# Performance work log

Hardware: AMD Instinct MI355X
Metric: run time of the kernel (lower is better)

The kernel has to match this reference:

```python
import jax, jax.numpy as jnp
import numpy as np
from jax import lax

LEAK = 0.2
GN_EPS = 1e-5
K_NEIGH = 16
GROUPS = 4


def knn_idx(coor_k, coor_q, k):
    # coor_k: [B,Nk,3], coor_q: [B,Nq,3] -> [B,Nq,k] indices of k nearest in coor_k
    d = (jnp.sum(coor_q * coor_q, -1, keepdims=True)
         - 2.0 * jnp.einsum('bqc,bkc->bqk', coor_q, coor_k)
         + jnp.sum(coor_k * coor_k, -1)[:, None, :])
    _, idx = lax.top_k(-d, k)
    return idx


def graph_feature(coor_q, x_q, coor_k, x_k, k):
    # coor_*: [B,3,N*]; x_q: [B,C,Nq]; x_k: [B,C,Nk] -> [B,2C,Nq,k]
    idx = knn_idx(lax.stop_gradient(coor_k).transpose(0, 2, 1),
                  lax.stop_gradient(coor_q).transpose(0, 2, 1), k)
    B = x_k.shape[0]
    x_k_t = x_k.transpose(0, 2, 1)                      # [B,Nk,C]
    b_idx = jnp.arange(B)[:, None, None]
    nb = x_k_t[b_idx, idx]                              # [B,Nq,k,C]
    nb = nb.transpose(0, 3, 1, 2)                       # [B,C,Nq,k]
    xq = x_q[:, :, :, None]                             # [B,C,Nq,1]
    return jnp.concatenate([nb - xq, jnp.broadcast_to(xq, nb.shape)], axis=1)


def conv_gn_lrelu_max(f, w, gamma, beta):
    # f: [B,Cin,N,k]; w: [Cout,Cin] -> [B,Cout,N] (max over k)
    y = jnp.einsum('oc,bcnk->bonk', w, f)
    B, C, N, Kk = y.shape
    g = y.reshape(B, GROUPS, C // GROUPS, N, Kk)
    mu = g.mean((2, 3, 4), keepdims=True)
    var = g.var((2, 3, 4), keepdims=True)
    g = (g - mu) * lax.rsqrt(var + GN_EPS)
    y = g.reshape(B, C, N, Kk) * gamma[None, :, None, None] + beta[None, :, None, None]
    y = jnp.where(y >= 0, y, LEAK * y)
    return y.max(axis=-1)


def fps(xyz, n):
    # xyz: [B,N,3] -> [B,n] int32 (furthest point sampling, start at index 0)
    B, N, _ = xyz.shape
    d0 = jnp.sum((xyz - xyz[:, :1]) ** 2, -1)           # dist to point 0
    def body(dist, _):
        idx = jnp.argmax(dist, -1)                       # [B]
        nxt = jnp.take_along_axis(xyz, idx[:, None, None], 1)
        dist = jnp.minimum(dist, jnp.sum((xyz - nxt) ** 2, -1))
        return dist, idx
    _, idxs = lax.scan(body, d0, None, length=n - 1)     # [n-1,B]
    first = jnp.zeros((1, B), idxs.dtype)
    return jnp.concatenate([first, idxs], 0).T           # [B,n]


def fps_downsample(coor, x, n):
    # coor: [B,3,N], x: [B,C,N] -> ([B,3,n], [B,C,n])
    idx = fps(lax.stop_gradient(coor).transpose(0, 2, 1), n)
    comb = jnp.concatenate([coor, x], axis=1)            # [B,3+C,N]
    b_idx = jnp.arange(coor.shape[0])[:, None]
    new = comb.transpose(0, 2, 1)[b_idx, idx].transpose(0, 2, 1)
    return new[:, :3], new[:, 3:]


def setup_inputs() -> dict:
    key = jax.random.key(0)
    ks = jax.random.split(key, 16)
    s = 0.1
    return {
        'x': jax.random.normal(ks[0], (32, 2048, 3), jnp.float32),
        'w_in': jax.random.normal(ks[1], (8, 3), jnp.float32) * s,
        'b_in': jnp.zeros((8,), jnp.float32),
        'w1': jax.random.normal(ks[2], (32, 16), jnp.float32) * s,
        'g1': jnp.ones((32,), jnp.float32), 'be1': jnp.zeros((32,), jnp.float32),
        'w2': jax.random.normal(ks[3], (64, 64), jnp.float32) * s,
        'g2': jnp.ones((64,), jnp.float32), 'be2': jnp.zeros((64,), jnp.float32),
        'w3': jax.random.normal(ks[4], (64, 128), jnp.float32) * s,
        'g3': jnp.ones((64,), jnp.float32), 'be3': jnp.zeros((64,), jnp.float32),
        'w4': jax.random.normal(ks[5], (256, 128), jnp.float32) * s,
        'g4': jnp.ones((256,), jnp.float32), 'be4': jnp.zeros((256,), jnp.float32),
        'num0': 512,
        'num1': 128,
    }


def reference(x, w_in, b_in, w1, g1, be1, w2, g2, be2, w3, g3, be3, w4, g4, be4, num0, num1):
    coor = x.transpose(0, 2, 1)                          # [B,3,N]
    f = jnp.einsum('oc,bcn->bon', w_in, coor) + b_in[None, :, None]  # input_trans
    f = graph_feature(coor, f, coor, f, K_NEIGH)         # [B,16,N,k]
    f = conv_gn_lrelu_max(f, w1, g1, be1)                # [B,32,N]
    coor_q, f_q = fps_downsample(coor, f, num0)
    f = graph_feature(coor_q, f_q, coor, f, K_NEIGH)     # [B,64,num0,k]
    f = conv_gn_lrelu_max(f, w2, g2, be2)                # [B,64,num0]
    coor = coor_q
    f = graph_feature(coor, f, coor, f, K_NEIGH)         # [B,128,num0,k]
    f = conv_gn_lrelu_max(f, w3, g3, be3)                # [B,64,num0]
    coor_q, f_q = fps_downsample(coor, f, num1)
    f = graph_feature(coor_q, f_q, coor, f, K_NEIGH)     # [B,128,num1,k]
    f = conv_gn_lrelu_max(f, w4, g4, be4)                # [B,256,num1]
    coor = coor_q
    return coor.transpose(0, 2, 1), f.transpose(0, 2, 1)  # [B,num1,3], [B,num1,256]
```

## Files before the change

### kernel.cpp

```cpp
#include <hip/hip_runtime.h>

#define BB 32
#define NPTS0 2048
#define KNB 16
#define KC 256

constexpr int ilog2c(int n){ int l=0; while(n>1){ n>>=1; ++l; } return l; }

static __device__ __forceinline__ float sq3(float a, float b, float c){
  return __fadd_rn(__fadd_rn(__fmul_rn(a,a),__fmul_rn(b,b)),__fmul_rn(c,c));
}

template<int CTRL, int RM>
static __device__ __forceinline__ float dpp_maxf(float v){
  int s = __builtin_amdgcn_update_dpp(__float_as_int(v), __float_as_int(v), CTRL, RM, 0xF, false);
  return fmaxf(v, __int_as_float(s));
}
template<int CTRL, int RM>
static __device__ __forceinline__ unsigned dpp_minu(unsigned v){
  unsigned s = (unsigned)__builtin_amdgcn_update_dpp((int)v, (int)v, CTRL, RM, 0xF, false);
  return s < v ? s : v;
}

static __device__ __forceinline__ void proj_body(const float* __restrict__ x,
    const float* __restrict__ w, const float* __restrict__ bias, float* __restrict__ f0,
    int blk)
{
  int gid = blk*256 + threadIdx.x;
  if (gid >= BB*NPTS0) return;
  float x0 = x[gid*3+0], x1 = x[gid*3+1], x2 = x[gid*3+2];
  #pragma unroll
  for (int o = 0; o < 8; ++o){
    float acc = __fmul_rn(w[o*3+0], x0);
    acc = __fmaf_rn(w[o*3+1], x1, acc);
    acc = __fmaf_rn(w[o*3+2], x2, acc);
    f0[gid*8+o] = __fadd_rn(acc, bias[o]);
  }
}

#define KDECL(I) float th##I = __builtin_inff(); int ti##I = 0;
#define KINS(I,J) if (th##I < th##J){ float tv=th##I; th##I=th##J; th##J=tv; \
                                      int tj=ti##I; ti##I=ti##J; ti##J=tj; }
#define KCASCADE KINS(15,14) KINS(14,13) KINS(13,12) KINS(12,11) KINS(11,10) \
  KINS(10,9) KINS(9,8) KINS(8,7) KINS(7,6) KINS(6,5) KINS(5,4) KINS(4,3) \
  KINS(3,2) KINS(2,1) KINS(1,0)
#define KALLDECL KDECL(0) KDECL(1) KDECL(2) KDECL(3) KDECL(4) KDECL(5) KDECL(6) KDECL(7) \
  KDECL(8) KDECL(9) KDECL(10) KDECL(11) KDECL(12) KDECL(13) KDECL(14) KDECL(15)
#define KST(I) pd[base+I] = th##I; pi[base+I] = (unsigned char)ti##I;
#define KST16(I) pd[base+I] = th##I; pi[base+I] = (unsigned short)ti##I;
#define MST(I) oidx[obase+I] = ti##I;

static __device__ __forceinline__ void knn_part512_body(const float* __restrict__ qpts,
    const float* __restrict__ kpts, int Nq, int Nk, int nkc,
    float* __restrict__ pd, unsigned short* __restrict__ pi,
    int b, int qcb, int kc, float4* kk4)
{
  int tid = threadIdx.x;
  int q = qcb*256 + tid;
  float qx = qpts[(b*Nq+q)*3+0], qy = qpts[(b*Nq+q)*3+1], qz = qpts[(b*Nq+q)*3+2];
  float qq = sq3(qx,qy,qz);
  KALLDECL
  #pragma unroll
  for (int half=0; half<2; ++half){
    __syncthreads();
    {
      int j = kc*512 + half*256 + tid;
      float a = kpts[(b*Nk+j)*3+0];
      float c = kpts[(b*Nk+j)*3+1];
      float dd = kpts[(b*Nk+j)*3+2];
      kk4[tid] = make_float4(a, c, dd, sq3(a,c,dd));
    }
    __syncthreads();
    for (int j=0;j<KC;j++){
      float4 k4 = kk4[j];
      float dot = __fmul_rn(qx,k4.x);
      dot = __fmaf_rn(qy,k4.y,dot);
      dot = __fmaf_rn(qz,k4.z,dot);
      float d = __fadd_rn(__fsub_rn(qq, __fmul_rn(2.0f,dot)), k4.w);
      if (d < th15){
        th15 = d; ti15 = half*256 + j;
        KCASCADE
      }
    }
  }
  size_t base = ((size_t)(b*Nq+q)*nkc + kc)*KNB;
  KST16(0) KST16(1) KST16(2) KST16(3) KST16(4) KST16(5) KST16(6) KST16(7)
  KST16(8) KST16(9) KST16(10) KST16(11) KST16(12) KST16(13) KST16(14) KST16(15)
}

static __device__ __forceinline__ void knn_part_body(const float* __restrict__ qpts,
    const float* __restrict__ kpts, int Nq, int Nk, int nkc,
    float* __restrict__ pd, unsigned char* __restrict__ pi,
    int b, int qcb, int kc, float4* kk4, const int* __restrict__ qidx, int NinQ)
{
  int tid = threadIdx.x;
  {
    int j = kc*KC + tid;
    float a = kpts[(b*Nk+j)*3+0];
    float c = kpts[(b*Nk+j)*3+1];
    float d = kpts[(b*Nk+j)*3+2];
    kk4[tid] = make_float4(a, c, d, sq3(a,c,d));
  }
  __syncthreads();
  int q = qcb*256 + tid;
  if (q >= Nq) return;
  int qrow = qidx ? (b*NinQ + qidx[b*Nq+q]) : (b*Nq+q);
  float qx = qpts[qrow*3+0], qy = qpts[qrow*3+1], qz = qpts[qrow*3+2];
  float qq = sq3(qx,qy,qz);
  KALLDECL
  for (int j=0;j<KC;j++){
    float4 k4 = kk4[j];
    float dot = __fmul_rn(qx,k4.x);
    dot = __fmaf_rn(qy,k4.y,dot);
    dot = __fmaf_rn(qz,k4.z,dot);
    float d = __fadd_rn(__fsub_rn(qq, __fmul_rn(2.0f,dot)), k4.w);
    if (d < th15){
      th15 = d; ti15 = j;
      KCASCADE
    }
  }
  size_t base = ((size_t)(b*Nq+q)*nkc + kc)*KNB;
  KST(0) KST(1) KST(2) KST(3) KST(4) KST(5) KST(6) KST(7)
  KST(8) KST(9) KST(10) KST(11) KST(12) KST(13) KST(14) KST(15)
}

static __device__ __forceinline__ void knn_merge_body(const float* __restrict__ pd,
    const unsigned char* __restrict__ pi, int Nq, int nkc, int* __restrict__ oidx,
    int blk)
{
  int gid = blk*256 + threadIdx.x;
  if (gid >= BB*Nq) return;
  KALLDECL
  size_t base = (size_t)gid*nkc*KNB;
  for (int kc=0;kc<nkc;kc++){
    size_t cb = base + (size_t)kc*KNB;
    for (int i=0;i<KNB;i++){
      float d = pd[cb+i];
      if (d >= th15) break;
      int j = kc*KC + (int)pi[cb+i];
      th15 = d; ti15 = j;
      KCASCADE
    }
  }
  int obase = gid*KNB;
  MST(0) MST(1) MST(2) MST(3) MST(4) MST(5) MST(6) MST(7)
  MST(8) MST(9) MST(10) MST(11) MST(12) MST(13) MST(14) MST(15)
}

static __device__ __forceinline__ void knn_merge512_body(const float* __restrict__ pd,
    const unsigned short* __restrict__ pi, int Nq, int nkc, int* __restrict__ oidx,
    int blk)
{
  int gid = blk*256 + threadIdx.x;
  if (gid >= BB*Nq) return;
  KALLDECL
  size_t base = (size_t)gid*nkc*KNB;
  for (int kc=0;kc<nkc;kc++){
    size_t cb = base + (size_t)kc*KNB;
    for (int i=0;i<KNB;i++){
      float d = pd[cb+i];
      if (d >= th15) break;
      int j = kc*512 + (int)pi[cb+i];
      th15 = d; ti15 = j;
      KCASCADE
    }
  }
  int obase = gid*KNB;
  MST(0) MST(1) MST(2) MST(3) MST(4) MST(5) MST(6) MST(7)
  MST(8) MST(9) MST(10) MST(11) MST(12) MST(13) MST(14) MST(15)
}

#define FPS_LOAD(T) float px##T, py##T, pz##T, d##T; { int i_=T*256+tid; \
  px##T=P[i_*3+0]; py##T=P[i_*3+1]; pz##T=P[i_*3+2]; \
  float dx_=__fsub_rn(px##T,c0x), dy_=__fsub_rn(py##T,c0y), dz_=__fsub_rn(pz##T,c0z); \
  d##T=sq3(dx_,dy_,dz_); bm=fmaxf(bm,d##T); }
#define FPS_MATCH(T) if (d##T == m_w) ci = (unsigned)(T*256 + tid);
#define FPS_OWN(T) if ((idx_w>>8) == T##u){ cx=px##T; cy=py##T; cz=pz##T; }
#define FPS_UPD(T) { float dx_=__fsub_rn(px##T,sx), dy_=__fsub_rn(py##T,sy), dz_=__fsub_rn(pz##T,sz); \
  float nd_=sq3(dx_,dy_,dz_); d##T=fminf(d##T,nd_); nbm=fmaxf(nbm,d##T); }

#define FPS_REDUCE_AND_PICK \
    float v = bm; \
    v = dpp_maxf<0x111, 0xF>(v); \
    v = dpp_maxf<0x112, 0xF>(v); \
    v = dpp_maxf<0x114, 0xF>(v); \
    v = dpp_maxf<0x118, 0xF>(v); \
    v = dpp_maxf<0x142, 0xA>(v); \
    v = dpp_maxf<0x143, 0xC>(v); \
    float m_w = __int_as_float(__builtin_amdgcn_readlane(__float_as_int(v), 63)); \
    unsigned ci = 0xFFFFFFFFu;

#define FPS_MIN_AND_MERGE \
    ci = dpp_minu<0x111, 0xF>(ci); \
    ci = dpp_minu<0x112, 0xF>(ci); \
    ci = dpp_minu<0x114, 0xF>(ci); \
    ci = dpp_minu<0x118, 0xF>(ci); \
    ci = dpp_minu<0x142, 0xA>(ci); \
    ci = dpp_minu<0x143, 0xC>(ci); \
    unsigned idx_w = (unsigned)__builtin_amdgcn_readlane((int)ci, 63); \
    int par = s & 1;

#define FPS_CROSSWAVE \
    __syncthreads(); \
    float4 q0 = *(const float4*)&swp[par][0][0]; float z0 = swp[par][0][4]; \
    float4 q1 = *(const float4*)&swp[par][1][0]; float z1 = swp[par][1][4]; \
    float4 q2 = *(const float4*)&swp[par][2][0]; float z2 = swp[par][2][4]; \
    float4 q3 = *(const float4*)&swp[par][3][0]; float z3 = swp[par][3][4]; \
    float mm = q0.x; unsigned mi = __float_as_uint(q0.y); \
    float sx = q0.z, sy = q0.w, sz = z0; \
    if (q1.x > mm || (q1.x == mm && __float_as_uint(q1.y) < mi)){ \
      mm = q1.x; mi = __float_as_uint(q1.y); sx = q1.z; sy = q1.w; sz = z1; } \
    if (q2.x > mm || (q2.x == mm && __float_as_uint(q2.y) < mi)){ \
      mm = q2.x; mi = __float_as_uint(q2.y); sx = q2.z; sy = q2.w; sz = z2; } \
    if (q3.x > mm || (q3.x == mm && __float_as_uint(q3.y) < mi)){ \
      mm = q3.x; mi = __float_as_uint(q3.y); sx = q3.z; sy = q3.w; sz = z3; } \
    if (tid == 0) oibuf[s] = (int)mi;

static __device__ __forceinline__ void fps8_body(const float* __restrict__ pts,
    int S, int* __restrict__ oidx, int b, char* smraw)
{
  float (*swp)[4][8] = reinterpret_cast<float(*)[4][8]>(smraw);
  int* oibuf = reinterpret_cast<int*>(smraw + 256);
  int tid = threadIdx.x, wid = tid >> 6;
  const float* P = pts + (size_t)b*2048*3;
  float c0x = P[0], c0y = P[1], c0z = P[2];
  float bm = -1.0f;
  FPS_LOAD(0) FPS_LOAD(1) FPS_LOAD(2) FPS_LOAD(3)
  FPS_LOAD(4) FPS_LOAD(5) FPS_LOAD(6) FPS_LOAD(7)
  if (tid == 0) oibuf[0] = 0;
  for (int s=1; s<S; ++s){
    FPS_REDUCE_AND_PICK
    FPS_MATCH(7) FPS_MATCH(6) FPS_MATCH(5) FPS_MATCH(4)
    FPS_MATCH(3) FPS_MATCH(2) FPS_MATCH(1) FPS_MATCH(0)
    FPS_MIN_AND_MERGE
    if (tid == (int)(idx_w & 255u)){
      float cx = px0, cy = py0, cz = pz0;
      FPS_OWN(1) FPS_OWN(2) FPS_OWN(3) FPS_OWN(4) FPS_OWN(5) FPS_OWN(6) FPS_OWN(7)
      float4* wp = (float4*)&swp[par][wid][0];
      *wp = make_float4(m_w, __uint_as_float(idx_w), cx, cy);
      swp[par][wid][4] = cz;
    }
    FPS_CROSSWAVE
    float nbm = -1.0f;
    FPS_UPD(0) FPS_UPD(1) FPS_UPD(2) FPS_UPD(3)
    FPS_UPD(4) FPS_UPD(5) FPS_UPD(6) FPS_UPD(7)
    bm = nbm;
  }
  __syncthreads();
  for (int s2 = tid; s2 < S; s2 += 256) oidx[b*S + s2] = oibuf[s2];
}

static __device__ __forceinline__ void fps2_body(const float* __restrict__ pts,
    int S, int* __restrict__ oidx, int b, char* smraw)
{
  float (*swp)[4][8] = reinterpret_cast<float(*)[4][8]>(smraw);
  int* oibuf = reinterpret_cast<int*>(smraw + 256);
  int tid = threadIdx.x, wid = tid >> 6;
  const float* P = pts + (size_t)b*512*3;
  float c0x = P[0], c0y = P[1], c0z = P[2];
  float bm = -1.0f;
  FPS_LOAD(0) FPS_LOAD(1)
  if (tid == 0) oibuf[0] = 0;
  for (int s=1; s<S; ++s){
    FPS_REDUCE_AND_PICK
    FPS_MATCH(1) FPS_MATCH(0)
    FPS_MIN_AND_MERGE
    if (tid == (int)(idx_w & 255u)){
      float cx = px0, cy = py0, cz = pz0;
      FPS_OWN(1)
      float4* wp = (float4*)&swp[par][wid][0];
      *wp = make_float4(m_w, __uint_as_float(idx_w), cx, cy);
      swp[par][wid][4] = cz;
    }
    FPS_CROSSWAVE
    float nbm = -1.0f;
    FPS_UPD(0) FPS_UPD(1)
    bm = nbm;
  }
  __syncthreads();
  for (int s2 = tid; s2 < S; s2 += 256) oidx[b*S + s2] = oibuf[s2];
}

template<int C, int O, bool DIFF>
static __device__ __forceinline__ void gemv_body(const float* __restrict__ fin,
    const float* __restrict__ W, float* __restrict__ out, int Npts, int blk)
{
  constexpr int NT = O/8;
  constexpr int LNT = ilog2c(NT);
  int gid = blk*256 + threadIdx.x;
  if (gid >= BB*Npts*NT) return;
  int tile = gid & (NT-1);
  int pn = gid >> LNT;
  const float* frow = fin + (size_t)pn*C;
  float f[C];
  #pragma unroll
  for (int c=0;c<C;c++) f[c] = frow[c];
  float acc[8];
  const float* wbase = W + (tile*8)*(2*C);
  #pragma unroll
  for (int oo=0;oo<8;oo++){
    const float* wrow = wbase + oo*(2*C);
    float a = 0.f;
    #pragma unroll
    for (int c=0;c<C;c++){
      float wv = DIFF ? __fsub_rn(wrow[C+c], wrow[c]) : wrow[c];
      a = __fmaf_rn(wv, f[c], a);
    }
    acc[oo] = a;
  }
  float* orow = out + (size_t)pn*O + tile*8;
  #pragma unroll
  for (int oo=0;oo<8;oo++) orow[oo] = acc[oo];
}

template<int C, int O, int LNB>
static __device__ __forceinline__ void gemv_bodyBind(const float* __restrict__ fin,
    const float* __restrict__ W, float* __restrict__ out, int blk,
    const int* __restrict__ gidx, int NinB)
{
  constexpr int NT = O/8;
  constexpr int LNT = ilog2c(NT);
  int gid = blk*256 + threadIdx.x;
  if (gid >= BB*(1<<LNB)*NT) return;
  int tile = gid & (NT-1);
  int pn = gid >> LNT;
  int b = pn >> LNB;
  int src = gidx[pn];
  const float* frow = fin + (size_t)(b*NinB + src)*C;
  float f[C];
  #pragma unroll
  for (int c=0;c<C;c++) f[c] = frow[c];
  float acc[8];
  const float* wbase = W + (tile*8)*(2*C);
  #pragma unroll
  for (int oo=0;oo<8;oo++){
    const float* wrow = wbase + oo*(2*C);
    float a = 0.f;
    #pragma unroll
    for (int c=0;c<C;c++){
      float wv = __fsub_rn(wrow[C+c], wrow[c]);
      a = __fmaf_rn(wv, f[c], a);
    }
    acc[oo] = a;
  }
  float* orow = out + (size_t)pn*O + tile*8;
  #pragma unroll
  for (int oo=0;oo<8;oo++) orow[oo] = acc[oo];
}

template<int C, int O, int LNB, bool BIND>
__global__ __launch_bounds__(256) void gemv_dual_kernel(const float* __restrict__ finA,
    const float* __restrict__ finB, const float* __restrict__ W,
    float* __restrict__ outA, float* __restrict__ outB,
    int NptsA, int NptsB, int nAblk, const int* __restrict__ gidxB, int NinB)
{
  int bid = blockIdx.x;
  if (bid < nAblk) gemv_body<C,O,false>(finA, W, outA, NptsA, bid);
  else if constexpr (BIND) gemv_bodyBind<C,O,LNB>(finB, W, outB, bid-nAblk, gidxB, NinB);
  else gemv_body<C,O,true>(finB, W, outB, NptsB, bid-nAblk);
}

template<int O>
static __device__ __forceinline__ void stats2_body(const float* __restrict__ A,
    const float* __restrict__ Bq, const int* __restrict__ idx, int Nq, int Nk,
    double* __restrict__ part, int b, int split, int nsplit, double* sh )
{
  constexpr int O4 = O/4;
  int qlen = Nq / nsplit, q0 = split*qlen;
  int tid = threadIdx.x;
  int pairs = qlen * KNB;
  double s1[4] = {0.0,0.0,0.0,0.0};
  double s2[4] = {0.0,0.0,0.0,0.0};
  for (int p = tid; p < pairs; p += 256){
    int q = q0 + (p >> 4);
    int kk = p & 15;
    int j = idx[(b*Nq+q)*KNB + kk];
    const float* arow = A + (size_t)(b*Nk+j)*O;
    const float* brow = Bq + (size_t)(b*Nq+q)*O;
    #pragma unroll
    for (int g=0; g<4; ++g){
      float cs1 = 0.f, cs2 = 0.f;
      #pragma unroll
      for (int c=0; c<O4; c+=4){
        float4 a4 = *(const float4*)(arow + g*O4 + c);
        float4 b4 = *(const float4*)(brow + g*O4 + c);
        float y0 = a4.x+b4.x, y1 = a4.y+b4.y, y2 = a4.z+b4.z, y3 = a4.w+b4.w;
        cs1 += ((y0+y1)+(y2+y3));
        cs2 = fmaf(y0,y0,cs2); cs2 = fmaf(y1,y1,cs2);
        cs2 = fmaf(y2,y2,cs2); cs2 = fmaf(y3,y3,cs2);
      }
      s1[g] += (double)cs1;
      s2[g] += (double)cs2;
    }
  }
  #pragma unroll
  for (int m=32;m>0;m>>=1){
    #pragma unroll
    for (int g=0; g<4; ++g){
      s1[g] += __shfl_down(s1[g], m);
      s2[g] += __shfl_down(s2[g], m);
    }
  }
  int lane = tid & 63, w = tid >> 6;
  if (lane == 0){
    #pragma unroll
    for (int g=0; g<4; ++g){ sh[w*8+g*2] = s1[g]; sh[w*8+g*2+1] = s2[g]; }
  }
  __syncthreads();
  if (tid == 0){
    #pragma unroll
    for (int g=0; g<4; ++g){
      double t1 = (sh[0*8+g*2]+sh[1*8+g*2]) + (sh[2*8+g*2]+sh[3*8+g*2]);
      double t2 = (sh[0*8+g*2+1]+sh[1*8+g*2+1]) + (sh[2*8+g*2+1]+sh[3*8+g*2+1]);
      int pi = (b*4+g)*nsplit + split;
      part[pi*2] = t1; part[pi*2+1] = t2;
    }
  }
}

template<int O>
__global__ __launch_bounds__(256) void stats2_kernel(const float* __restrict__ A,
    const float* __restrict__ Bq, const int* __restrict__ idx, int Nq, int Nk,
    double* __restrict__ part)
{
  __shared__ double sh[32];
  stats2_body<O>(A, Bq, idx, Nq, Nk, part, blockIdx.x, blockIdx.y, gridDim.y, sh);
}

template<int O>
__global__ __launch_bounds__(256) void final_kernel(const float* __restrict__ A,
    const float* __restrict__ Bq, const int* __restrict__ idx,
    const double* __restrict__ part, int nsplit, double cnt,
    const float* __restrict__ gamma, const float* __restrict__ beta,
    float* __restrict__ fout, int Nq, int Nk)
{
  constexpr int LO = ilog2c(O);
  constexpr int LO4 = ilog2c(O/4);
  __shared__ float smu[4], srs[4];
  int b = blockIdx.y;
  if (threadIdx.x < 4){
    int g = threadIdx.x;
    int t0 = b*4+g;
    double s1=0.0, s2=0.0;
    for (int i=0;i<nsplit;i++){ s1 += part[(t0*nsplit+i)*2]; s2 += part[(t0*nsplit+i)*2+1]; }
    double mean = s1/cnt;
    double var = s2/cnt - mean*mean;
    double rstd = 1.0 / sqrt(var + 1e-5);
    smu[g] = (float)mean;
    srs[g] = (float)rstd;
  }
  __syncthreads();
  int t = blockIdx.x*256 + threadIdx.x;
  if (t >= Nq*O) return;
  int o = t & (O-1);
  int q = t >> LO;
  int g = o >> LO4;
  float mu   = smu[g];
  float rstd = srs[g];
  float gam = gamma[o], bet = beta[o];
  float bq = Bq[(b*Nq+q)*O + o];
  const int* ip = idx + (b*Nq+q)*KNB;
  float m = -__builtin_inff();
  #pragma unroll
  for (int kk=0;kk<KNB;kk++){
    int j = ip[kk];
    float y = A[(b*Nk+j)*O + o] + bq;
    float yn = __fmul_rn(__fsub_rn(y, mu), rstd);
    float yv = __fadd_rn(__fmul_rn(yn, gam), bet);
    float l = yv >= 0.f ? yv : 0.2f*yv;
    m = fmaxf(m, l);
  }
  fout[(b*Nq+q)*O + o] = m;
}

static __device__ __forceinline__ void gatherc_body(const int* __restrict__ fidx,
    const float* __restrict__ pts, float* __restrict__ cq, int Nin, int Nout, int blk)
{
  int gid = blk*256 + threadIdx.x;
  if (gid >= BB*Nout) return;
  int b = gid / Nout;
  int i = gid - b*Nout;
  int src = fidx[b*Nout + i];
  #pragma unroll
  for (int c=0;c<3;c++) cq[gid*3+c] = pts[(b*Nin+src)*3+c];
}

__global__ __launch_bounds__(256) void gatherc_kernel(const int* __restrict__ fidx,
    const float* __restrict__ pts, float* __restrict__ cq, int Nin, int Nout)
{
  gatherc_body(fidx, pts, cq, Nin, Nout, blockIdx.x);
}

__global__ __launch_bounds__(256) void fused1_kernel(const float* __restrict__ x,
    const float* __restrict__ w_in, const float* __restrict__ b_in,
    float* __restrict__ f0, float* __restrict__ pd1, unsigned short* __restrict__ pi1,
    int* __restrict__ fidx0)
{
  __shared__ __align__(16) char sm[4096];
  int bid = blockIdx.x;
  if (bid < 32){
    __builtin_amdgcn_s_setprio(3);
    fps8_body(x, 512, fidx0, bid, sm);
  } else if (bid < 32+1024){
    int r = bid - 32;
    int b = r & 31; int rest = r >> 5;
    knn_part512_body(x, x, 2048, 2048, 4, pd1, pi1, b, rest & 7, rest >> 3, (float4*)sm);
  } else {
    proj_body(x, w_in, b_in, f0, bid - 1056);
  }
}

__global__ __launch_bounds__(256) void fused2_kernel(const float* __restrict__ coorq1,
    const float* __restrict__ x,
    float* __restrict__ pd2, unsigned char* __restrict__ pi2,
    float* __restrict__ pd3, unsigned char* __restrict__ pi3,
    int* __restrict__ fidx1,
    const float* __restrict__ pd1, const unsigned short* __restrict__ pi1,
    int* __restrict__ idx1,
    const float* __restrict__ f0, const float* __restrict__ w1,
    float* __restrict__ A1, float* __restrict__ B1)
{
  __shared__ __align__(16) char sm[4096];
  int bid = blockIdx.x;
  if (bid < 32){
    __builtin_amdgcn_s_setprio(3);
    fps2_body(coorq1, 128, fidx1, bid, sm);
  } else if (bid < 32+512){
    int r = bid - 32;
    int b = r & 31; int rest = r >> 5;
    knn_part_body(coorq1, x, 512, 2048, 8, pd2, pi2, b, rest & 1, rest >> 1,
                  (float4*)sm, nullptr, 0);
  } else if (bid < 32+512+128){
    int r = bid - 544;
    int b = r & 31; int rest = r >> 5;
    knn_part_body(coorq1, coorq1, 512, 512, 2, pd3, pi3, b, rest & 1, rest >> 1,
                  (float4*)sm, nullptr, 0);
  } else if (bid < 928){
    knn_merge512_body(pd1, pi1, 2048, 4, idx1, bid - 672);
  } else if (bid < 1952){
    gemv_body<8,32,false>(f0, w1, A1, 2048, bid - 928);
  } else {
    gemv_body<8,32,true>(f0, w1, B1, 2048, bid - 1952);
  }
}

__global__ __launch_bounds__(256) void fused3_kernel(
    const float* __restrict__ A1, const float* __restrict__ B1,
    const int* __restrict__ idx1, double* __restrict__ part,
    const float* __restrict__ pd2, const unsigned char* __restrict__ pi2, int* __restrict__ idx2,
    const float* __restrict__ pd3, const unsigned char* __restrict__ pi3, int* __restrict__ idx3,
    const float* __restrict__ coorq1, const int* __restrict__ fidx1,
    float* __restrict__ pd4, unsigned char* __restrict__ pi4,
    float* __restrict__ coor_out)
{
  __shared__ __align__(16) char sm[4096];
  int bid = blockIdx.x;
  if (bid < 256){
    stats2_body<32>(A1, B1, idx1, 2048, 2048, part, bid >> 3, bid & 7, 8, (double*)sm);
  } else if (bid < 320){
    knn_merge_body(pd2, pi2, 512, 8, idx2, bid - 256);
  } else if (bid < 384){
    knn_merge_body(pd3, pi3, 512, 2, idx3, bid - 320);
  } else if (bid < 448){
    int r = bid - 384;
    int b = r & 31; int kc = r >> 5;
    knn_part_body(coorq1, coorq1, 128, 512, 2, pd4, pi4, b, 0, kc,
                  (float4*)sm, fidx1, 512);
  } else {
    gatherc_body(fidx1, coorq1, coor_out, 512, 128, bid - 448);
  }
}

__global__ __launch_bounds__(256) void fused4_kernel(const float* __restrict__ f1,
    const float* __restrict__ w2, float* __restrict__ A, float* __restrict__ Bq,
    const int* __restrict__ fidx0,
    const float* __restrict__ pd4, const unsigned char* __restrict__ pi4,
    int* __restrict__ idx4)
{
  int bid = blockIdx.x;
  if (bid < 2048) gemv_body<32,64,false>(f1, w2, A, 2048, bid);
  else if (bid < 2560) gemv_bodyBind<32,64,9>(f1, w2, Bq, bid - 2048, fidx0, 2048);
  else knn_merge_body(pd4, pi4, 128, 2, idx4, bid - 2560);
}

extern "C" void kernel_launch(void* const* d_in, const int* in_sizes, int n_in,
                              void* d_out, int out_size, void* d_ws, size_t ws_size,
                              hipStream_t stream)
{
  (void)in_sizes; (void)n_in; (void)out_size; (void)ws_size;
  const float* x    = (const float*)d_in[0];
  const float* w_in = (const float*)d_in[1];
  const float* b_in = (const float*)d_in[2];
  const float* w1 = (const float*)d_in[3];
  const float* g1 = (const float*)d_in[4];
  const float* be1= (const float*)d_in[5];
  const float* w2 = (const float*)d_in[6];
  const float* g2 = (const float*)d_in[7];
  const float* be2= (const float*)d_in[8];
  const float* w3 = (const float*)d_in[9];
  const float* g3 = (const float*)d_in[10];
  const float* be3= (const float*)d_in[11];
  const float* w4 = (const float*)d_in[12];
  const float* g4 = (const float*)d_in[13];
  const float* be4= (const float*)d_in[14];

  float* out = (float*)d_out;
  float* coor_out = out;
  float* f_out = out + BB*128*3;

  char* ws = (char*)d_ws;
  size_t off = 0;
  auto alloc = [&](size_t bytes)->void*{ void* p = ws + off; off += (bytes + 255) & ~(size_t)255; return p; };

  float* f0     = (float*)alloc((size_t)BB*2048*8*4);
  int*   idx1   = (int*)  alloc((size_t)BB*2048*16*4);
  float* f1     = (float*)alloc((size_t)BB*2048*32*4);
  double* part  = (double*)alloc((size_t)BB*4*8*2*8);
  int*   fidx0  = (int*)  alloc((size_t)BB*512*4);
  float* coorq1 = (float*)alloc((size_t)BB*512*3*4);
  int*   idx2   = (int*)  alloc((size_t)BB*512*16*4);
  float* f2     = (float*)alloc((size_t)BB*512*64*4);
  int*   idx3   = (int*)  alloc((size_t)BB*512*16*4);
  float* f3     = (float*)alloc((size_t)BB*512*64*4);
  int*   fidx1  = (int*)  alloc((size_t)BB*128*4);
  int*   idx4   = (int*)  alloc((size_t)BB*128*16*4);
  float* pd2          = (float*)alloc((size_t)BB*512*8*KNB*4);
  unsigned char* pi2  = (unsigned char*)alloc((size_t)BB*512*8*KNB);
  float* pd3          = (float*)alloc((size_t)BB*512*2*KNB*4);
  unsigned char* pi3  = (unsigned char*)alloc((size_t)BB*512*2*KNB);
  float* pd4          = (float*)alloc((size_t)BB*128*2*KNB*4);
  unsigned char* pi4  = (unsigned char*)alloc((size_t)BB*128*2*KNB);

  char* U = (char*)alloc((size_t)40<<20);
  float* pd1          = (float*)U;
  unsigned short* pi1 = (unsigned short*)(U + ((size_t)16<<20));
  float* A1 = (float*)(U + ((size_t)24<<20));
  float* B1 = (float*)(U + ((size_t)32<<20));
  float* A  = (float*)U;
  float* Bq = (float*)(U + ((size_t)20<<20));

  auto cdiv = [](int a, int b){ return (a+b-1)/b; };

  fused1_kernel<<<1312,256,0,stream>>>(x, w_in, b_in, f0, pd1, pi1, fidx0);
  gatherc_kernel<<<cdiv(BB*512,256),256,0,stream>>>(fidx0, x, coorq1, 2048, 512);
  fused2_kernel<<<2976,256,0,stream>>>(coorq1, x, pd2, pi2, pd3, pi3, fidx1,
                                       pd1, pi1, idx1, f0, w1, A1, B1);
  fused3_kernel<<<464,256,0,stream>>>(A1, B1, idx1, part, pd2, pi2, idx2,
                                      pd3, pi3, idx3, coorq1, fidx1, pd4, pi4, coor_out);
  final_kernel<32><<<dim3(cdiv(2048*32,256),BB),256,0,stream>>>(A1, B1, idx1, part, 8,
      8.0*2048*16, g1, be1, f1, 2048, 2048);
  fused4_kernel<<<2576,256,0,stream>>>(f1, w2, A, Bq, fidx0, pd4, pi4, idx4);
  stats2_kernel<64><<<dim3(BB,8),256,0,stream>>>(A, Bq, idx2, 512, 2048, part);
  final_kernel<64><<<dim3(cdiv(512*64,256),BB),256,0,stream>>>(A, Bq, idx2, part, 8,
      16.0*512*16, g2, be2, f2, 512, 2048);
  gemv_dual_kernel<64,64,0,false><<<1024,256,0,stream>>>(f2, f2, w3, A, Bq,
      512, 512, 512, nullptr, 0);
  stats2_kernel<64><<<dim3(BB,8),256,0,stream>>>(A, Bq, idx3, 512, 512, part);
  final_kernel<64><<<dim3(cdiv(512*64,256),BB),256,0,stream>>>(A, Bq, idx3, part, 8,
      16.0*512*16, g3, be3, f3, 512, 512);
  gemv_dual_kernel<64,256,7,true><<<2560,256,0,stream>>>(f3, f3, w4, A, Bq,
      512, 128, 2048, fidx1, 512);
  stats2_kernel<256><<<dim3(BB,8),256,0,stream>>>(A, Bq, idx4, 128, 512, part);
  final_kernel<256><<<dim3(cdiv(128*256,256),BB),256,0,stream>>>(A, Bq, idx4, part, 8,
      64.0*128*16, g4, be4, f_out, 128, 512);
}
```

Before: 1.218 ms.

## Track per-channel neighbor max/min in stats pass so final skips regather

The stats kernel now loops over neighbors per query and channel chunk, accumulating sums for group-norm statistics while also recording per-channel max and min of the pre-norm values. The final kernel applies the affine normalization and leaky ReLU only to the max or the min, picked by the sign of gamma, since the transform is monotone. This removes the second 16-way gather of neighbor rows in the final pass, at the cost of writing and reading two extra [Nq,O] buffers. Scratch-buffer offsets are reshuffled to fit the new arrays.

```diff
diff --git a/kernel.cpp b/kernel.cpp
--- a/kernel.cpp
+++ b/kernel.cpp
@@ -361,50 +361,54 @@
 }
 
 template<int O>
-static __device__ __forceinline__ void stats2_body(const float* __restrict__ A,
+static __device__ __forceinline__ void statsmm_body(const float* __restrict__ A,
     const float* __restrict__ Bq, const int* __restrict__ idx, int Nq, int Nk,
-    double* __restrict__ part, int b, int split, int nsplit, double* sh )
-{
-  constexpr int O4 = O/4;
+    double* __restrict__ part, float* __restrict__ ymax, float* __restrict__ ymin,
+    int b, int split, int nsplit, double* sh )
+{
+  constexpr int NCH = O/4;
+  constexpr int LNCH = ilog2c(NCH);
+  constexpr int W = NCH/4;
   int qlen = Nq / nsplit, q0 = split*qlen;
   int tid = threadIdx.x;
-  int pairs = qlen * KNB;
-  double s1[4] = {0.0,0.0,0.0,0.0};
-  double s2[4] = {0.0,0.0,0.0,0.0};
-  for (int p = tid; p < pairs; p += 256){
-    int q = q0 + (p >> 4);
-    int kk = p & 15;
-    int j = idx[(b*Nq+q)*KNB + kk];
-    const float* arow = A + (size_t)(b*Nk+j)*O;
-    const float* brow = Bq + (size_t)(b*Nq+q)*O;
+  int items = qlen * NCH;
+  double s1 = 0.0, s2 = 0.0;
+  for (int p = tid; p < items; p += 256){
+    int q = q0 + (p >> LNCH);
+    int ch = p & (NCH-1);
+    const int* ip = idx + (b*Nq+q)*KNB;
+    size_t yo = (size_t)(b*Nq+q)*O + ch*4;
+    float4 b4 = *(const float4*)(Bq + yo);
+    float mx0=-__builtin_inff(), mx1=mx0, mx2=mx0, mx3=mx0;
+    float mn0= __builtin_inff(), mn1=mn0, mn2=mn0, mn3=mn0;
+    float cs1 = 0.f, cs2 = 0.f;
     #pragma unroll
-    for (int g=0; g<4; ++g){
-      float cs1 = 0.f, cs2 = 0.f;
-      #pragma unroll
-      for (int c=0; c<O4; c+=4){
-        float4 a4 = *(const float4*)(arow + g*O4 + c);
-        float4 b4 = *(const float4*)(brow + g*O4 + c);
-        float y0 = a4.x+b4.x, y1 = a4.y+b4.y, y2 = a4.z+b4.z, y3 = a4.w+b4.w;
-        cs1 += ((y0+y1)+(y2+y3));
-        cs2 = fmaf(y0,y0,cs2); cs2 = fmaf(y1,y1,cs2);
-        cs2 = fmaf(y2,y2,cs2); cs2 = fmaf(y3,y3,cs2);
-      }
-      s1[g] += (double)cs1;
-      s2[g] += (double)cs2;
-    }
-  }
-  #pragma unroll
-  for (int m=32;m>0;m>>=1){
-    #pragma unroll
-    for (int g=0; g<4; ++g){
-      s1[g] += __shfl_down(s1[g], m);
-      s2[g] += __shfl_down(s2[g], m);
-    }
-  }
-  int lane = tid & 63, w = tid >> 6;
-  if (lane == 0){
-    #pragma unroll
-    for (int g=0; g<4; ++g){ sh[w*8+g*2] = s1[g]; sh[w*8+g*2+1] = s2[g]; }
+    for (int kk=0; kk<KNB; ++kk){
+      int j = ip[kk];
+      float4 a4 = *(const float4*)(A + (size_t)(b*Nk+j)*O + ch*4);
+      float y0 = a4.x+b4.x, y1 = a4.y+b4.y, y2 = a4.z+b4.z, y3 = a4.w+b4.w;
+      cs1 += ((y0+y1)+(y2+y3));
+      cs2 = fmaf(y0,y0,cs2); cs2 = fmaf(y1,y1,cs2);
+      cs2 = fmaf(y2,y2,cs2); cs2 = fmaf(y3,y3,cs2);
+      mx0=fmaxf(mx0,y0); mx1=fmaxf(mx1,y1); mx2=fmaxf(mx2,y2); mx3=fmaxf(mx3,y3);
+      mn0=fminf(mn0,y0); mn1=fminf(mn1,y1); mn2=fminf(mn2,y2); mn3=fminf(mn3,y3);
+    }
+    *(float4*)(ymax + yo) = make_float4(mx0,mx1,mx2,mx3);
+    *(float4*)(ymin + yo) = make_float4(mn0,mn1,mn2,mn3);
+    s1 += (double)cs1;
+    s2 += (double)cs2;
+  }
+  if constexpr (W >= 2){ s1 += __shfl_xor(s1,1);  s2 += __shfl_xor(s2,1);  }
+  if constexpr (W >= 4){ s1 += __shfl_xor(s1,2);  s2 += __shfl_xor(s2,2);  }
+  if constexpr (W >= 8){ s1 += __shfl_xor(s1,4);  s2 += __shfl_xor(s2,4);  }
+  if constexpr (W >= 16){ s1 += __shfl_xor(s1,8); s2 += __shfl_xor(s2,8);  }
+  if constexpr (NCH <= 8){  s1 += __shfl_xor(s1,8);  s2 += __shfl_xor(s2,8);  }
+  if constexpr (NCH <= 16){ s1 += __shfl_xor(s1,16); s2 += __shfl_xor(s2,16); }
+  if constexpr (NCH <= 32){ s1 += __shfl_xor(s1,32); s2 += __shfl_xor(s2,32); }
+  int lane = tid & 63, wv = tid >> 6;
+  if (lane < NCH && (lane & (W-1)) == 0){
+    int g = lane / W;
+    sh[wv*8+g*2] = s1; sh[wv*8+g*2+1] = s2;
   }
   __syncthreads();
   if (tid == 0){
@@ -419,20 +423,21 @@
 }
 
 template<int O>
-__global__ __launch_bounds__(256) void stats2_kernel(const float* __restrict__ A,
+__global__ __launch_bounds__(256) void statsmm_kernel(const float* __restrict__ A,
     const float* __restrict__ Bq, const int* __restrict__ idx, int Nq, int Nk,
-    double* __restrict__ part)
+    double* __restrict__ part, float* __restrict__ ymax, float* __restrict__ ymin)
 {
   __shared__ double sh[32];
-  stats2_body<O>(A, Bq, idx, Nq, Nk, part, blockIdx.x, blockIdx.y, gridDim.y, sh);
+  statsmm_body<O>(A, Bq, idx, Nq, Nk, part, ymax, ymin,
+                  blockIdx.x, blockIdx.y, gridDim.y, sh);
 }
 
 template<int O>
-__global__ __launch_bounds__(256) void final_kernel(const float* __restrict__ A,
-    const float* __restrict__ Bq, const int* __restrict__ idx,
+__global__ __launch_bounds__(256) void final_kernel(
+    const float* __restrict__ ymax, const float* __restrict__ ymin,
     const double* __restrict__ part, int nsplit, double cnt,
     const float* __restrict__ gamma, const float* __restrict__ beta,
-    float* __restrict__ fout, int Nq, int Nk)
+    float* __restrict__ fout, int Nq)
 {
   constexpr int LO = ilog2c(O);
   constexpr int LO4 = ilog2c(O/4);
@@ -455,22 +460,12 @@
   int o = t & (O-1);
   int q = t >> LO;
   int g = o >> LO4;
-  float mu   = smu[g];
-  float rstd = srs[g];
   float gam = gamma[o], bet = beta[o];
-  float bq = Bq[(b*Nq+q)*O + o];
-  const int* ip = idx + (b*Nq+q)*KNB;
-  float m = -__builtin_inff();
-  #pragma unroll
-  for (int kk=0;kk<KNB;kk++){
-    int j = ip[kk];
-    float y = A[(b*Nk+j)*O + o] + bq;
-    float yn = __fmul_rn(__fsub_rn(y, mu), rstd);
-    float yv = __fadd_rn(__fmul_rn(yn, gam), bet);
-    float l = yv >= 0.f ? yv : 0.2f*yv;
-    m = fmaxf(m, l);
-  }
-  fout[(b*Nq+q)*O + o] = m;
+  size_t yo = (size_t)(b*Nq+q)*O + o;
+  float ysel = (gam >= 0.f) ? ymax[yo] : ymin[yo];
+  float yn = __fmul_rn(__fsub_rn(ysel, smu[g]), srs[g]);
+  float yv = __fadd_rn(__fmul_rn(yn, gam), bet);
+  fout[yo] = yv >= 0.f ? yv : 0.2f*yv;
 }
 
 static __device__ __forceinline__ void gatherc_body(const int* __restrict__ fidx,
@@ -547,6 +542,7 @@
 __global__ __launch_bounds__(256) void fused3_kernel(
     const float* __restrict__ A1, const float* __restrict__ B1,
     const int* __restrict__ idx1, double* __restrict__ part,
+    float* __restrict__ ymax, float* __restrict__ ymin,
     const float* __restrict__ pd2, const unsigned char* __restrict__ pi2, int* __restrict__ idx2,
     const float* __restrict__ pd3, const unsigned char* __restrict__ pi3, int* __restrict__ idx3,
     const float* __restrict__ coorq1, const int* __restrict__ fidx1,
@@ -556,7 +552,8 @@
   __shared__ __align__(16) char sm[4096];
   int bid = blockIdx.x;
   if (bid < 256){
-    stats2_body<32>(A1, B1, idx1, 2048, 2048, part, bid >> 3, bid & 7, 8, (double*)sm);
+    statsmm_body<32>(A1, B1, idx1, 2048, 2048, part, ymax, ymin,
+                     bid >> 3, bid & 7, 8, (double*)sm);
   } else if (bid < 320){
     knn_merge_body(pd2, pi2, 512, 8, idx2, bid - 256);
   } else if (bid < 384){
@@ -636,8 +633,10 @@
   unsigned short* pi1 = (unsigned short*)(U + ((size_t)16<<20));
   float* A1 = (float*)(U + ((size_t)24<<20));
   float* B1 = (float*)(U + ((size_t)32<<20));
-  float* A  = (float*)U;
-  float* Bq = (float*)(U + ((size_t)20<<20));
+  float* ymax = (float*)U;
+  float* ymin = (float*)(U + ((size_t)8<<20));
+  float* A  = (float*)(U + ((size_t)16<<20));
+  float* Bq = (float*)(U + ((size_t)32<<20));
 
   auto cdiv = [](int a, int b){ return (a+b-1)/b; };
 
@@ -645,22 +644,23 @@
   gatherc_kernel<<<cdiv(BB*512,256),256,0,stream>>>(fidx0, x, coorq1, 2048, 512);
   fused2_kernel<<<2976,256,0,stream>>>(coorq1, x, pd2, pi2, pd3, pi3, fidx1,
                                        pd1, pi1, idx1, f0, w1, A1, B1);
-  fused3_kernel<<<464,256,0,stream>>>(A1, B1, idx1, part, pd2, pi2, idx2,
-                                      pd3, pi3, idx3, coorq1, fidx1, pd4, pi4, coor_out);
-  final_kernel<32><<<dim3(cdiv(2048*32,256),BB),256,0,stream>>>(A1, B1, idx1, part, 8,
-      8.0*2048*16, g1, be1, f1, 2048, 2048);
+  fused3_kernel<<<464,256,0,stream>>>(A1, B1, idx1, part, ymax, ymin,
+                                      pd2, pi2, idx2, pd3, pi3, idx3,
+                                      coorq1, fidx1, pd4, pi4, coor_out);
+  final_kernel<32><<<dim3(cdiv(2048*32,256),BB),256,0,stream>>>(ymax, ymin, part, 8,
+      8.0*2048*16, g1, be1, f1, 2048);
   fused4_kernel<<<2576,256,0,stream>>>(f1, w2, A, Bq, fidx0, pd4, pi4, idx4);
-  stats2_kernel<64><<<dim3(BB,8),256,0,stream>>>(A, Bq, idx2, 512, 2048, part);
-  final_kernel<64><<<dim3(cdiv(512*64,256),BB),256,0,stream>>>(A, Bq, idx2, part, 8,
-      16.0*512*16, g2, be2, f2, 512, 2048);
+  statsmm_kernel<64><<<dim3(BB,8),256,0,stream>>>(A, Bq, idx2, 512, 2048, part, ymax, ymin);
+  final_kernel<64><<<dim3(cdiv(512*64,256),BB),256,0,stream>>>(ymax, ymin, part, 8,
+      16.0*512*16, g2, be2, f2, 512);
   gemv_dual_kernel<64,64,0,false><<<1024,256,0,stream>>>(f2, f2, w3, A, Bq,
       512, 512, 512, nullptr, 0);
-  stats2_kernel<64><<<dim3(BB,8),256,0,stream>>>(A, Bq, idx3, 512, 512, part);
-  final_kernel<64><<<dim3(cdiv(512*64,256),BB),256,0,stream>>>(A, Bq, idx3, part, 8,
-      16.0*512*16, g3, be3, f3, 512, 512);
+  statsmm_kernel<64><<<dim3(BB,8),256,0,stream>>>(A, Bq, idx3, 512, 512, part, ymax, ymin);
+  final_kernel<64><<<dim3(cdiv(512*64,256),BB),256,0,stream>>>(ymax, ymin, part, 8,
+      16.0*512*16, g3, be3, f3, 512);
   gemv_dual_kernel<64,256,7,true><<<2560,256,0,stream>>>(f3, f3, w4, A, Bq,
       512, 128, 2048, fidx1, 512);
-  stats2_kernel<256><<<dim3(BB,8),256,0,stream>>>(A, Bq, idx4, 128, 512, part);
-  final_kernel<256><<<dim3(cdiv(128*256,256),BB),256,0,stream>>>(A, Bq, idx4, part, 8,
-      64.0*128*16, g4, be4, f_out, 128, 512);
-}
+  statsmm_kernel<256><<<dim3(BB,8),256,0,stream>>>(A, Bq, idx4, 128, 512, part, ymax, ymin);
+  final_kernel<256><<<dim3(cdiv(128*256,256),BB),256,0,stream>>>(ymax, ymin, part, 8,
+      64.0*128*16, g4, be4, f_out, 128);
+}
```

Result: no change. 1.196 ms (median of 2 runs) (-1.8%).
